# Performance work log

Hardware: AMD Instinct MI355X
Metric: run time of the kernel (lower is better)

The kernel has to match this reference:

```python
import jax, jax.numpy as jnp
import numpy as np

NUM_CONTROL_POINTS = 4
# Standard Catmull-Rom spline basis (rows map [1, t, t^2, t^3] monomials to control points)
CATMULL_ROM_BASIS = 0.5 * np.array(
    [[0.0, 2.0, 0.0, 0.0],
     [-1.0, 0.0, 1.0, 0.0],
     [2.0, -5.0, 4.0, -1.0],
     [-1.0, 3.0, -3.0, 1.0]], dtype=np.float32)

BATCH, IN_F, OUT_F = 1024, 512, 512


def setup_inputs() -> dict:
    key = jax.random.key(0)
    k1, k2, k3, k4 = jax.random.split(key, 4)
    inp = jax.random.normal(k1, (BATCH, IN_F), dtype=jnp.float32)
    # phase spans [0, 2*pi) so both spline segments (mask = phase < 1.5*pi) are exercised
    phase = jax.random.uniform(k2, (BATCH,), dtype=jnp.float32) * (2.0 * jnp.pi)
    bound = 1.0 / np.sqrt(IN_F)
    weights = jax.random.uniform(k3, (NUM_CONTROL_POINTS, OUT_F, IN_F), dtype=jnp.float32,
                                 minval=-bound, maxval=bound)
    biases = jax.random.uniform(k4, (NUM_CONTROL_POINTS, OUT_F), dtype=jnp.float32,
                                minval=-bound, maxval=bound)
    return {"input": inp, "phase": phase, "weights": weights, "biases": biases}


def _spline_coeffs(phase):
    # Faithful to the original (including its overwrite bug): tt = [1, t^2, t^3, 0]
    basis = jnp.asarray(CATMULL_ROM_BASIS, dtype=phase.dtype)
    t0 = phase / (1.5 * jnp.pi)
    t1 = (phase - 0.5 * jnp.pi) / (1.5 * jnp.pi)
    ones, zeros = jnp.ones_like(phase), jnp.zeros_like(phase)
    tt0 = jnp.stack([ones, t0 * t0, t0 ** 3, zeros], axis=1)  # (B,4)
    tt1 = jnp.stack([ones, t1 * t1, t1 ** 3, zeros], axis=1)  # (B,4)
    mask = (phase < 1.5 * jnp.pi)[:, None]
    # Selecting per-sample coefficients before the weight contraction is exactly
    # equivalent to where(mask, tt0@B@W, tt1@B@W) since the map is linear in tt.
    return jnp.where(mask, tt0 @ basis, tt1 @ basis)  # (B,4) control-point coeffs


def reference(input, phase, weights, biases):
    c = _spline_coeffs(phase)                       # (B,4)
    # Fused form: apply the 4 shared control-point linear layers, then blend,
    # avoiding the (B,out,in) per-sample weight tensor. Same math as
    # (tt@B@W).reshape(B,out,in) @ input[:,:,None] + b.
    y4 = jnp.einsum('bi,coi->bco', input, weights)  # (B,4,out)
    out = jnp.einsum('bc,bco->bo', c, y4) + c @ biases  # (B,out)
    return out
```

## Files before the change

kernel.cpp:

```cpp
#include <hip/hip_runtime.h>


#define BATCH 1024
#define IN_F  512
#define OUT_F 512

typedef unsigned short u16;
typedef u16    u16x8  __attribute__((ext_vector_type(8)));
typedef __bf16 bf16x8 __attribute__((ext_vector_type(8)));
typedef float  f32x4  __attribute__((ext_vector_type(4)));

#define A_GRANULES 65536
#define W_GRANULES 131072

__device__ __forceinline__ u16 f2bits(float f) {
  union { float f; unsigned int u; } v; v.f = f;
  unsigned int u = v.u;
  unsigned int r = u + 0x7fffu + ((u >> 16) & 1u);
  return (u16)(r >> 16);
}

__global__ __launch_bounds__(256)
void Convert_kernel(const float* __restrict__ inp, const float* __restrict__ wts,
                    u16x8* __restrict__ ws) {
  const int s = blockIdx.x * 256 + threadIdx.x;
  const float* src;
  if (s < A_GRANULES) {
    const int frag = s >> 6, l = s & 63;
    const int btile = frag >> 4, kblk = frag & 15;
    const int m = l & 15, qq = l >> 4;
    src = inp + (size_t)(btile * 16 + m) * IN_F + kblk * 32 + qq * 8;
  } else {
    const int t = s - A_GRANULES;
    const int frag = t >> 6, l = t & 63;
    const int kblk = frag & 15, rest = frag >> 4;
    const int c = rest & 3, otile = rest >> 2;
    const int n = l & 15, qq = l >> 4;
    src = wts + ((size_t)c * OUT_F + otile * 16 + n) * IN_F + kblk * 32 + qq * 8;
  }
  const f32x4 v0 = *(const f32x4*)src;
  const f32x4 v1 = *(const f32x4*)(src + 4);
  u16x8 pk;
#pragma unroll
  for (int x = 0; x < 4; ++x) {
    pk[x]     = f2bits(v0[x]);
    pk[x + 4] = f2bits(v1[x]);
  }
  ws[s] = pk;
}

__global__ __launch_bounds__(128)
void PhaseLinear_kernel(const u16x8* __restrict__ ws, const float* __restrict__ ph,
                        const float* __restrict__ bia, float* __restrict__ outp) {
  __shared__ f32x4 sRed[8][64];

  const int tid = threadIdx.x;
  const int ks  = tid >> 6;
  const int l   = tid & 63;
  const int q   = l >> 4;
  const int n   = l & 15;
  const int otile = blockIdx.x;
  const int bty   = blockIdx.y;

  const bf16x8* __restrict__ A  = (const bf16x8*)ws;
  const bf16x8* __restrict__ Wp = (const bf16x8*)ws + A_GRANULES;

  const int ai0 = ((bty * 2 + 0) * 16 + ks * 8) * 64 + l;
  const int ai1 = ((bty * 2 + 1) * 16 + ks * 8) * 64 + l;
  int wi[4];
#pragma unroll
  for (int c = 0; c < 4; ++c) wi[c] = ((otile * 4 + c) * 16 + ks * 8) * 64 + l;

  bf16x8 a[2][2], w[2][4];
  a[0][0] = A[ai0];
  a[0][1] = A[ai1];
#pragma unroll
  for (int c = 0; c < 4; ++c) w[0][c] = Wp[wi[c]];

  f32x4 acc[2][4];
#pragma unroll
  for (int mi = 0; mi < 2; ++mi)
#pragma unroll
    for (int c = 0; c < 4; ++c) acc[mi][c] = (f32x4){0.f, 0.f, 0.f, 0.f};

#pragma unroll
  for (int kk = 0; kk < 8; ++kk) {
    const int cb = kk & 1, nb = cb ^ 1;
    if (kk < 7) {
      const int off = (kk + 1) * 64;
      a[nb][0] = A[ai0 + off];
      a[nb][1] = A[ai1 + off];
#pragma unroll
      for (int c = 0; c < 4; ++c) w[nb][c] = Wp[wi[c] + off];
    }
#pragma unroll
    for (int mi = 0; mi < 2; ++mi)
#pragma unroll
      for (int c = 0; c < 4; ++c)
        acc[mi][c] = __builtin_amdgcn_mfma_f32_16x16x32_bf16(a[cb][mi], w[cb][c],
                                                             acc[mi][c], 0, 0, 0);
  }

  if (ks == 1) {
#pragma unroll
    for (int mi = 0; mi < 2; ++mi)
#pragma unroll
      for (int c = 0; c < 4; ++c) sRed[mi * 4 + c][l] = acc[mi][c];
  }
  __syncthreads();

  if (ks == 0) {
    const float PI = 3.14159265358979323846f;
    const int o = otile * 16 + n;
    float bs[4];
#pragma unroll
    for (int c = 0; c < 4; ++c) bs[c] = bia[c * OUT_F + o];

#pragma unroll
    for (int mi = 0; mi < 2; ++mi) {
#pragma unroll
      for (int r = 0; r < 4; ++r) {
        const int b = bty * 32 + mi * 16 + q * 4 + r;
        const float p  = ph[b];
        const float t  = (p < 1.5f * PI) ? (p / (1.5f * PI)) : ((p - 0.5f * PI) / (1.5f * PI));
        const float t2 = t * t, t3 = t2 * t;
        const float c0 = t3 - 0.5f * t2;
        const float c1 = 1.0f - 2.5f * t3;
        const float c2 = 0.5f * t2 + 2.0f * t3;
        const float c3 = -0.5f * t3;
        const float s0 = acc[mi][0][r] + sRed[mi * 4 + 0][l][r];
        const float s1 = acc[mi][1][r] + sRed[mi * 4 + 1][l][r];
        const float s2 = acc[mi][2][r] + sRed[mi * 4 + 2][l][r];
        const float s3 = acc[mi][3][r] + sRed[mi * 4 + 3][l][r];
        outp[(size_t)b * OUT_F + o] =
            c0 * (s0 + bs[0]) + c1 * (s1 + bs[1]) + c2 * (s2 + bs[2]) + c3 * (s3 + bs[3]);
      }
    }
  }
}

extern "C" void kernel_launch(void* const* d_in, const int* in_sizes, int n_in,
                              void* d_out, int out_size, void* d_ws, size_t ws_size,
                              hipStream_t stream) {
  const float* inp = (const float*)d_in[0];
  const float* ph  = (const float*)d_in[1];
  const float* wts = (const float*)d_in[2];
  const float* bia = (const float*)d_in[3];
  float* outp = (float*)d_out;

  Convert_kernel<<<dim3((A_GRANULES + W_GRANULES) / 256), 256, 0, stream>>>(
      inp, wts, (u16x8*)d_ws);

  dim3 grid(OUT_F / 16, BATCH / 32);
  PhaseLinear_kernel<<<grid, 128, 0, stream>>>((const u16x8*)d_ws, ph, bia, outp);
}
```

Before: 70.54 us.

## Enlarge batch tile to 64 and split K across four waves

Each block now covers 64 batch rows instead of 32, so every loaded weight fragment feeds four M-tiles and global weight traffic per output is halved. The K dimension is split across four waves of 128 each rather than two waves of 256, and three partial accumulators are reduced through a larger shared buffer. The grid shrinks to half as many blocks of 256 threads, with more accumulator registers and shared memory per block. The risks are lower occupancy and a heavier cross-wave reduction.

```diff
diff --git a/kernel.cpp b/kernel.cpp
--- a/kernel.cpp
+++ b/kernel.cpp
@@ -49,10 +49,10 @@
   ws[s] = pk;
 }
 
-__global__ __launch_bounds__(128)
+__global__ __launch_bounds__(256)
 void PhaseLinear_kernel(const u16x8* __restrict__ ws, const float* __restrict__ ph,
                         const float* __restrict__ bia, float* __restrict__ outp) {
-  __shared__ f32x4 sRed[8][64];
+  __shared__ f32x4 sRed[3][16][64];
 
   const int tid = threadIdx.x;
   const int ks  = tid >> 6;
@@ -65,47 +65,47 @@
   const bf16x8* __restrict__ A  = (const bf16x8*)ws;
   const bf16x8* __restrict__ Wp = (const bf16x8*)ws + A_GRANULES;
 
-  const int ai0 = ((bty * 2 + 0) * 16 + ks * 8) * 64 + l;
-  const int ai1 = ((bty * 2 + 1) * 16 + ks * 8) * 64 + l;
-  int wi[4];
+  int ai[4], wi[4];
 #pragma unroll
-  for (int c = 0; c < 4; ++c) wi[c] = ((otile * 4 + c) * 16 + ks * 8) * 64 + l;
+  for (int mi = 0; mi < 4; ++mi) ai[mi] = ((bty * 4 + mi) * 16 + ks * 4) * 64 + l;
+#pragma unroll
+  for (int c = 0; c < 4; ++c)    wi[c]  = ((otile * 4 + c) * 16 + ks * 4) * 64 + l;
 
-  bf16x8 a[2][2], w[2][4];
-  a[0][0] = A[ai0];
-  a[0][1] = A[ai1];
+  bf16x8 a[2][4], w[2][4];
 #pragma unroll
-  for (int c = 0; c < 4; ++c) w[0][c] = Wp[wi[c]];
+  for (int mi = 0; mi < 4; ++mi) a[0][mi] = A[ai[mi]];
+#pragma unroll
+  for (int c = 0; c < 4; ++c)    w[0][c]  = Wp[wi[c]];
 
-  f32x4 acc[2][4];
+  f32x4 acc[4][4];
 #pragma unroll
-  for (int mi = 0; mi < 2; ++mi)
+  for (int mi = 0; mi < 4; ++mi)
 #pragma unroll
     for (int c = 0; c < 4; ++c) acc[mi][c] = (f32x4){0.f, 0.f, 0.f, 0.f};
 
 #pragma unroll
-  for (int kk = 0; kk < 8; ++kk) {
+  for (int kk = 0; kk < 4; ++kk) {
     const int cb = kk & 1, nb = cb ^ 1;
-    if (kk < 7) {
+    if (kk < 3) {
       const int off = (kk + 1) * 64;
-      a[nb][0] = A[ai0 + off];
-      a[nb][1] = A[ai1 + off];
 #pragma unroll
-      for (int c = 0; c < 4; ++c) w[nb][c] = Wp[wi[c] + off];
+      for (int mi = 0; mi < 4; ++mi) a[nb][mi] = A[ai[mi] + off];
+#pragma unroll
+      for (int c = 0; c < 4; ++c)    w[nb][c]  = Wp[wi[c] + off];
     }
 #pragma unroll
-    for (int mi = 0; mi < 2; ++mi)
+    for (int mi = 0; mi < 4; ++mi)
 #pragma unroll
       for (int c = 0; c < 4; ++c)
         acc[mi][c] = __builtin_amdgcn_mfma_f32_16x16x32_bf16(a[cb][mi], w[cb][c],
                                                              acc[mi][c], 0, 0, 0);
   }
 
-  if (ks == 1) {
+  if (ks != 0) {
 #pragma unroll
-    for (int mi = 0; mi < 2; ++mi)
+    for (int mi = 0; mi < 4; ++mi)
 #pragma unroll
-      for (int c = 0; c < 4; ++c) sRed[mi * 4 + c][l] = acc[mi][c];
+      for (int c = 0; c < 4; ++c) sRed[ks - 1][mi * 4 + c][l] = acc[mi][c];
   }
   __syncthreads();
 
@@ -117,10 +117,17 @@
     for (int c = 0; c < 4; ++c) bs[c] = bia[c * OUT_F + o];
 
 #pragma unroll
-    for (int mi = 0; mi < 2; ++mi) {
+    for (int mi = 0; mi < 4; ++mi) {
+      f32x4 s[4];
+#pragma unroll
+      for (int c = 0; c < 4; ++c) {
+        s[c] = acc[mi][c];
+#pragma unroll
+        for (int j = 0; j < 3; ++j) s[c] += sRed[j][mi * 4 + c][l];
+      }
 #pragma unroll
       for (int r = 0; r < 4; ++r) {
-        const int b = bty * 32 + mi * 16 + q * 4 + r;
+        const int b = bty * 64 + mi * 16 + q * 4 + r;
         const float p  = ph[b];
         const float t  = (p < 1.5f * PI) ? (p / (1.5f * PI)) : ((p - 0.5f * PI) / (1.5f * PI));
         const float t2 = t * t, t3 = t2 * t;
@@ -128,12 +135,9 @@
         const float c1 = 1.0f - 2.5f * t3;
         const float c2 = 0.5f * t2 + 2.0f * t3;
         const float c3 = -0.5f * t3;
-        const float s0 = acc[mi][0][r] + sRed[mi * 4 + 0][l][r];
-        const float s1 = acc[mi][1][r] + sRed[mi * 4 + 1][l][r];
-        const float s2 = acc[mi][2][r] + sRed[mi * 4 + 2][l][r];
-        const float s3 = acc[mi][3][r] + sRed[mi * 4 + 3][l][r];
         outp[(size_t)b * OUT_F + o] =
-            c0 * (s0 + bs[0]) + c1 * (s1 + bs[1]) + c2 * (s2 + bs[2]) + c3 * (s3 + bs[3]);
+            c0 * (s[0][r] + bs[0]) + c1 * (s[1][r] + bs[1]) +
+            c2 * (s[2][r] + bs[2]) + c3 * (s[3][r] + bs[3]);
       }
     }
   }
@@ -151,6 +155,6 @@
   Convert_kernel<<<dim3((A_GRANULES + W_GRANULES) / 256), 256, 0, stream>>>(
       inp, wts, (u16x8*)d_ws);
 
-  dim3 grid(OUT_F / 16, BATCH / 32);
-  PhaseLinear_kernel<<<grid, 128, 0, stream>>>((const u16x8*)d_ws, ph, bia, outp);
+  dim3 grid(OUT_F / 16, BATCH / 64);
+  PhaseLinear_kernel<<<grid, 256, 0, stream>>>((const u16x8*)d_ws, ph, bia, outp);
 }
```

New measurement: 71.05 us. About the same (+0.7%).
